# Kernel tuning notes

Measured on AMD Instinct MI355X. Metric: run time of the kernel, lower is better.

## Reference

```python
import jax, jax.numpy as jnp
import numpy as np

B, C, H, W = 16, 96, 96, 96
K, N, R, CR = 4, 8, 6, 12  # scan dirs, d_state, dt_rank, SE hidden


def channel_ln(x, g, b, eps=1e-6):
    # LayerNorm over channel dim (channel_first)
    mu = jnp.mean(x, axis=1, keepdims=True)
    var = jnp.var(x, axis=1, keepdims=True)
    return (x - mu) * jax.lax.rsqrt(var + eps) * g[None, :, None, None] + b[None, :, None, None]


def conv1x1(x, w, b):
    return jnp.einsum('bchw,dc->bdhw', x, w) + b[None, :, None, None]


def ss2d(x, xproj_w, dtproj_w, dtproj_b, A_logs, Ds, g, bta):
    # 4-direction selective scan (VMamba SS2D core). x: (B,C,H,W)
    Bq, Cq, Hq, Wq = x.shape
    L = Hq * Wq
    xf = x.reshape(Bq, Cq, L)
    xt = jnp.transpose(x, (0, 1, 3, 2)).reshape(Bq, Cq, L)
    xs = jnp.stack([xf, xt, xf[..., ::-1], xt[..., ::-1]], axis=1)  # (B,K,C,L)
    x_dbl = jnp.einsum('bkcl,kdc->bkdl', xs, xproj_w)  # (B,K,R+2N,L)
    dts, Bs, Cs = jnp.split(x_dbl, [R, R + N], axis=2)
    delta = jax.nn.softplus(jnp.einsum('bkrl,kcr->bkcl', dts, dtproj_w) + dtproj_b[None, :, :, None])
    A = -jnp.exp(A_logs)  # (K,C,N)
    u_t = jnp.moveaxis(xs, -1, 0)   # (L,B,K,C)
    d_t = jnp.moveaxis(delta, -1, 0)
    B_t = jnp.moveaxis(Bs, -1, 0)   # (L,B,K,N)
    C_t = jnp.moveaxis(Cs, -1, 0)
    h0 = jnp.zeros((Bq, K, Cq, N), x.dtype)

    @jax.checkpoint
    def step(h, inp):
        u, d, Bv, Cv = inp
        dA = jnp.exp(d[..., None] * A)                      # (B,K,C,N)
        h = dA * h + (d * u)[..., None] * Bv[:, :, None, :]
        return h, jnp.sum(h * Cv[:, :, None, :], axis=-1)   # (B,K,C)

    _, ys = jax.lax.scan(step, h0, (u_t, d_t, B_t, C_t))
    ys = jnp.moveaxis(ys, 0, -1) + Ds[None, :, :, None] * xs  # (B,K,C,L)

    def untrans(yk):
        return jnp.transpose(yk.reshape(Bq, Cq, Wq, Hq), (0, 1, 3, 2)).reshape(Bq, Cq, L)

    out = ys[:, 0] + untrans(ys[:, 1]) + ys[:, 2, :, ::-1] + untrans(ys[:, 3][..., ::-1])
    return channel_ln(out.reshape(Bq, Cq, Hq, Wq), g, bta)


def block_forward(x, ln_g, ln_b, p1_w, p1_b, p2in_w, p2in_b, dw_w, dw_b,
                  xproj_w, dtproj_w, dtproj_b, A_logs, Ds, ssln_g, ssln_b,
                  p2n_g, p2n_b, ca_w1, ca_b1, ca_w2, ca_b2, block_idx):
    h = channel_ln(x, ln_g, ln_b)
    a = jax.nn.silu(conv1x1(h, p1_w, p1_b))
    z = conv1x1(h, p2in_w, p2in_b)
    z = jax.lax.conv_general_dilated(z, dw_w, (1, 1), 'SAME',
                                     dimension_numbers=('NCHW', 'OIHW', 'NCHW'),
                                     feature_group_count=z.shape[1]) + dw_b[None, :, None, None]
    z = jax.nn.silu(z)
    if block_idx % 2 == 0:
        z = jnp.transpose(z, (0, 1, 3, 2))
    else:
        z = z[:, :, ::-1, ::-1]
    z = ss2d(z, xproj_w, dtproj_w, dtproj_b, A_logs, Ds, ssln_g, ssln_b)
    if block_idx % 2 == 0:
        z = jnp.transpose(z, (0, 1, 3, 2))
    else:
        z = z[:, :, ::-1, ::-1]
    z = channel_ln(z, p2n_g, p2n_b)
    y = a * z
    # channel attention (SE)
    s = jnp.mean(y, axis=(2, 3))  # (B,C)
    att = jax.nn.sigmoid(jnp.einsum('cr,br->bc', ca_w2,
                                    jax.nn.silu(jnp.einsum('rc,bc->br', ca_w1, s) + ca_b1)) + ca_b2)
    return x + y * att[:, :, None, None]


def local_mamba(x, params, block_idx):
    b, c, h, w = x.shape
    h2, w2 = h // 2, w // 2
    qs = jnp.stack([x[:, :, :h2, :w2], x[:, :, :h2, w2:],
                    x[:, :, h2:, :w2], x[:, :, h2:, w2:]])  # (4,B,C,h2,w2)
    fn = lambda q, *p: block_forward(q, *p, block_idx)
    outs = jax.vmap(fn)(qs, *params)
    top = jnp.concatenate([outs[0], outs[1]], axis=3)
    bot = jnp.concatenate([outs[2], outs[3]], axis=3)
    return jnp.concatenate([top, bot], axis=2)


def setup_inputs() -> dict:
    key = jax.random.key(0)
    ks = jax.random.split(key, 12)
    rn = lambda k, shape, s=1.0: jax.random.normal(k, shape, jnp.float32) * s
    return dict(
        x=rn(ks[0], (B, C, H, W)),
        ln_g=jnp.ones((4, C)), ln_b=jnp.zeros((4, C)),
        p1_w=rn(ks[1], (4, C, C), C ** -0.5), p1_b=jnp.zeros((4, C)),
        p2in_w=rn(ks[2], (4, C, C), C ** -0.5), p2in_b=jnp.zeros((4, C)),
        dw_w=rn(ks[3], (4, C, 1, 3, 3), 1.0 / 3.0), dw_b=jnp.zeros((4, C)),
        xproj_w=rn(ks[4], (4, K, R + 2 * N, C), C ** -0.5),
        dtproj_w=rn(ks[5], (4, K, C, R), R ** -0.5),
        dtproj_b=rn(ks[6], (4, K, C), 0.1),
        A_logs=jax.random.uniform(ks[7], (4, K, C, N), jnp.float32, 0.0, 1.0),
        Ds=jnp.ones((4, K, C)),
        ssln_g=jnp.ones((4, C)), ssln_b=jnp.zeros((4, C)),
        p2n_g=jnp.ones((4, C)), p2n_b=jnp.zeros((4, C)),
        ca_w1=rn(ks[8], (4, CR, C), C ** -0.5), ca_b1=jnp.zeros((4, CR)),
        ca_w2=rn(ks[9], (4, C, CR), CR ** -0.5), ca_b2=jnp.zeros((4, C)),
        block_idx=0,
    )


def reference(x, ln_g, ln_b, p1_w, p1_b, p2in_w, p2in_b, dw_w, dw_b,
              xproj_w, dtproj_w, dtproj_b, A_logs, Ds, ssln_g, ssln_b,
              p2n_g, p2n_b, ca_w1, ca_b1, ca_w2, ca_b2, block_idx):
    params = (ln_g, ln_b, p1_w, p1_b, p2in_w, p2in_b, dw_w, dw_b,
              xproj_w, dtproj_w, dtproj_b, A_logs, Ds, ssln_g, ssln_b,
              p2n_g, p2n_b, ca_w1, ca_b1, ca_w2, ca_b2)
    return local_mamba(x, params, block_idx)
```

## Files before the change

kernel.cpp:

```cpp
#include <hip/hip_runtime.h>
#include <hip/hip_bf16.h>

#define BQ 16
#define CN 96
#define HQ 48
#define LL 2304
#define NK 4
#define RR 6
#define NNS 8
#define DPJ 22
#define CRr 12
#define LOG2E 1.4426950408889634f

using bf16 = __hip_bfloat16;

__device__ __forceinline__ float b2f(bf16 v) { return __bfloat162float(v); }
__device__ __forceinline__ bf16  f2b(float v){ return __float2bfloat16(v); }
__device__ __forceinline__ float bflo(unsigned u){ return __uint_as_float(u << 16); }
__device__ __forceinline__ float bfhi(unsigned u){ return __uint_as_float(u & 0xffff0000u); }
__device__ __forceinline__ float sigf(float x){ return 1.f / (1.f + __expf(-x)); }
__device__ __forceinline__ float siluf(float x){ return x / (1.f + __expf(-x)); }
__device__ __forceinline__ unsigned packbf(float a, float b){
    unsigned lo = (unsigned)__builtin_bit_cast(unsigned short, f2b(a));
    unsigned hi = (unsigned)__builtin_bit_cast(unsigned short, f2b(b));
    return lo | (hi << 16);
}
__device__ __forceinline__ unsigned rot16(unsigned u){ return (u >> 16) | (u << 16); }
__device__ __forceinline__ void unpack8(uint4 v, float* f){
    f[0]=bflo(v.x); f[1]=bfhi(v.x); f[2]=bflo(v.y); f[3]=bfhi(v.y);
    f[4]=bflo(v.z); f[5]=bfhi(v.z); f[6]=bflo(v.w); f[7]=bfhi(v.w);
}
__device__ __forceinline__ void unpack4(uint2 v, float* f){
    f[0]=bflo(v.x); f[1]=bfhi(v.x); f[2]=bflo(v.y); f[3]=bfhi(v.y);
}
__device__ __forceinline__ float fexp2(float x){
#if __has_builtin(__builtin_amdgcn_exp2f)
    return __builtin_amdgcn_exp2f(x);
#else
    return __expf(x * 0.6931471805599453f);
#endif
}
__device__ __forceinline__ float qxor(float v, int ctrl_b1){
    int x;
    if (ctrl_b1) x = __builtin_amdgcn_mov_dpp(__float_as_int(v), 0xB1, 0xF, 0xF, true);
    else         x = __builtin_amdgcn_mov_dpp(__float_as_int(v), 0x4E, 0xF, 0xF, true);
    return __int_as_float(x);
}

__global__ __launch_bounds__(192) void k_lnconv(
    const float* __restrict__ x, const float* __restrict__ ln_g, const float* __restrict__ ln_b,
    const float* __restrict__ p1w, const float* __restrict__ p1b,
    const float* __restrict__ p2w, const float* __restrict__ p2b,
    bf16* __restrict__ a_out, bf16* __restrict__ z0_out)
{
    const int hh2 = blockIdx.x;
    const int b = blockIdx.y, q = blockIdx.z;
    const int h0 = (q >> 1) * HQ, w0 = (q & 1) * HQ;
    const int tid = threadIdx.x;
    const int qb = q * BQ + b;

    __shared__ alignas(16) bf16 hn[CN * 96];
    __shared__ alignas(16) bf16 wl[CN * 200];
    __shared__ float mu[96], rs[96];

    for (int t = tid; t < CN * CN; t += 192) {
        int d = t / CN, c = t % CN;
        wl[c * 200 + d]      = f2b(p1w[(q * CN + d) * CN + c]);
        wl[c * 200 + 96 + d] = f2b(p2w[(q * CN + d) * CN + c]);
    }
    for (int t = tid; t < CN * 24; t += 192) {
        int c = t / 24, v = t % 24;
        int row = v / 12, col = (v % 12) * 4;
        float4 xv = *reinterpret_cast<const float4*>(
            &x[((b * CN + c) * 96 + h0 + 2 * hh2 + row) * 96 + w0 + col]);
        uint2 pk; pk.x = packbf(xv.x, xv.y); pk.y = packbf(xv.z, xv.w);
        *reinterpret_cast<uint2*>(&hn[c * 96 + v * 4]) = pk;
    }
    __syncthreads();
    if (tid < 96) {
        float s = 0.f, s2 = 0.f;
        for (int c = 0; c < CN; ++c) { float v = b2f(hn[c * 96 + tid]); s += v; s2 += v * v; }
        float m = s * (1.f / 96.f);
        float var = s2 * (1.f / 96.f) - m * m;
        mu[tid] = m; rs[tid] = rsqrtf(var + 1e-6f);
    }
    __syncthreads();
    for (int t = tid; t < CN * 96; t += 192) {
        int c = t / 96, p = t % 96;
        float g = ln_g[q * CN + c], bb = ln_b[q * CN + c];
        hn[t] = f2b((b2f(hn[t]) - mu[p]) * rs[p] * g + bb);
    }
    __syncthreads();
    const int rg = tid >> 3, pg = tid & 7;
    const int row0 = rg * 8, pp0 = pg * 12;
    float acc[8][12];
    #pragma unroll
    for (int i = 0; i < 8; ++i)
        #pragma unroll
        for (int j = 0; j < 12; ++j) acc[i][j] = 0.f;

    for (int c = 0; c < CN; ++c) {
        uint4 wv = *reinterpret_cast<const uint4*>(&wl[c * 200 + row0]);
        float w[8];
        w[0] = bflo(wv.x); w[1] = bfhi(wv.x);
        w[2] = bflo(wv.y); w[3] = bfhi(wv.y);
        w[4] = bflo(wv.z); w[5] = bfhi(wv.z);
        w[6] = bflo(wv.w); w[7] = bfhi(wv.w);
        uint2 ha = *reinterpret_cast<const uint2*>(&hn[c * 96 + pp0]);
        uint2 hb = *reinterpret_cast<const uint2*>(&hn[c * 96 + pp0 + 4]);
        uint2 hc = *reinterpret_cast<const uint2*>(&hn[c * 96 + pp0 + 8]);
        float hv[12];
        hv[0] = bflo(ha.x); hv[1] = bfhi(ha.x); hv[2]  = bflo(ha.y); hv[3]  = bfhi(ha.y);
        hv[4] = bflo(hb.x); hv[5] = bfhi(hb.x); hv[6]  = bflo(hb.y); hv[7]  = bfhi(hb.y);
        hv[8] = bflo(hc.x); hv[9] = bfhi(hc.x); hv[10] = bflo(hc.y); hv[11] = bfhi(hc.y);
        #pragma unroll
        for (int i = 0; i < 8; ++i)
            #pragma unroll
            for (int j = 0; j < 12; ++j)
                acc[i][j] = fmaf(w[i], hv[j], acc[i][j]);
    }
    const int lbase = (2 * hh2 + pp0 / 48) * 48 + (pp0 % 48);
    #pragma unroll
    for (int i = 0; i < 8; ++i) {
        int row = row0 + i;
        bool isA = row < 96;
        int d = isA ? row : row - 96;
        float bias = isA ? p1b[q * CN + d] : p2b[q * CN + d];
        int oidx = (qb * CN + d) * LL + lbase;
        float v[12];
        #pragma unroll
        for (int j = 0; j < 12; ++j) v[j] = acc[i][j] + bias;
        if (isA) {
            #pragma unroll
            for (int j = 0; j < 12; ++j) v[j] = siluf(v[j]);
        }
        uint2 w0p, w1p, w2p;
        w0p.x = packbf(v[0], v[1]);  w0p.y = packbf(v[2], v[3]);
        w1p.x = packbf(v[4], v[5]);  w1p.y = packbf(v[6], v[7]);
        w2p.x = packbf(v[8], v[9]);  w2p.y = packbf(v[10], v[11]);
        bf16* dst = isA ? a_out : z0_out;
        *reinterpret_cast<uint2*>(&dst[oidx])     = w0p;
        *reinterpret_cast<uint2*>(&dst[oidx + 4]) = w1p;
        *reinterpret_cast<uint2*>(&dst[oidx + 8]) = w2p;
    }
}

__global__ __launch_bounds__(256) void k_dwconv(
    const bf16* __restrict__ z0, const float* __restrict__ dww, const float* __restrict__ dwb,
    const int* __restrict__ bidx, bf16* __restrict__ zt, bf16* __restrict__ ztT)
{
    const int c = blockIdx.x, b = blockIdx.y, q = blockIdx.z;
    const int tid = threadIdx.x;
    const int base = ((q * BQ + b) * CN + c) * LL;
    __shared__ float zin[LL];
    __shared__ float zo[48 * 49];
    for (int t = tid; t < 288; t += 256) {
        uint4 v = *reinterpret_cast<const uint4*>(&z0[base + t * 8]);
        float f[8]; unpack8(v, f);
        *reinterpret_cast<float4*>(&zin[t * 8])     = make_float4(f[0], f[1], f[2], f[3]);
        *reinterpret_cast<float4*>(&zin[t * 8 + 4]) = make_float4(f[4], f[5], f[6], f[7]);
    }
    float wk[9];
    #pragma unroll
    for (int i = 0; i < 9; ++i) wk[i] = dww[(q * CN + c) * 9 + i];
    const float bias = dwb[q * CN + c];
    __syncthreads();
    for (int t = tid; t < LL; t += 256) {
        int hh = t / 48, ww = t % 48;
        float s = bias;
        #pragma unroll
        for (int dy = -1; dy <= 1; ++dy)
            #pragma unroll
            for (int dx = -1; dx <= 1; ++dx) {
                int yy = hh + dy, xx = ww + dx;
                if (yy >= 0 && yy < 48 && xx >= 0 && xx < 48)
                    s = fmaf(wk[(dy + 1) * 3 + (dx + 1)], zin[yy * 48 + xx], s);
            }
        zo[hh * 49 + ww] = siluf(s);
    }
    __syncthreads();
    const bool even = ((bidx[0] & 1) == 0);
    for (int t = tid; t < LL; t += 256) {
        int i = t / 48, j = t % 48;
        float vz, vzT;
        if (even) { vz = zo[j * 49 + i];               vzT = zo[i * 49 + j]; }
        else      { vz = zo[(47 - i) * 49 + (47 - j)]; vzT = zo[(47 - j) * 49 + (47 - i)]; }
        zt[base + t]  = f2b(vz);
        ztT[base + t] = f2b(vzT);
    }
}

__global__ __launch_bounds__(256) void k_xdbl(
    const bf16* __restrict__ zt, const bf16* __restrict__ ztT,
    const float* __restrict__ xprojw, bf16* __restrict__ xdbl)
{
    const int lt = blockIdx.x, k = blockIdx.y, qb = blockIdx.z;
    const int tid = threadIdx.x;
    const int l0 = lt * 192;
    const int q = qb >> 4;
    __shared__ alignas(16) bf16 ul[CN * 200];
    __shared__ alignas(16) bf16 wl[CN * 24];
    const bf16* __restrict__ src = (k & 1) ? ztT : zt;
    const bool rev = (k >= 2);
    for (int t = tid; t < CN * 24; t += 256) {
        int cc = t / 24, j0 = (t % 24) * 8;
        uint4 v;
        if (!rev) {
            v = *reinterpret_cast<const uint4*>(&src[(size_t)(qb * CN + cc) * LL + l0 + j0]);
        } else {
            v = *reinterpret_cast<const uint4*>(&src[(size_t)(qb * CN + cc) * LL + (LL - (l0 + j0) - 8)]);
            uint4 r; r.x = rot16(v.w); r.y = rot16(v.z); r.z = rot16(v.y); r.w = rot16(v.x);
            v = r;
        }
        *reinterpret_cast<uint4*>(&ul[cc * 200 + j0]) = v;
    }
    for (int t = tid; t < DPJ * CN; t += 256) {
        int d = t / CN, c = t % CN;
        wl[c * 24 + d] = f2b(xprojw[(q * NK + k) * DPJ * CN + t]);
    }
    __syncthreads();
    if (tid < 176) {
        const int dp = tid / 16, lg = tid % 16;
        const int d0 = dp * 2, llp = lg * 12;
        float acc0[12], acc1[12];
        #pragma unroll
        for (int j = 0; j < 12; ++j) { acc0[j] = 0.f; acc1[j] = 0.f; }
        for (int c = 0; c < CN; ++c) {
            unsigned wv = *reinterpret_cast<const unsigned*>(&wl[c * 24 + d0]);
            float w0 = bflo(wv), w1 = bfhi(wv);
            uint2 ua = *reinterpret_cast<const uint2*>(&ul[c * 200 + llp]);
            uint2 ub = *reinterpret_cast<const uint2*>(&ul[c * 200 + llp + 4]);
            uint2 uc = *reinterpret_cast<const uint2*>(&ul[c * 200 + llp + 8]);
            float uf[12];
            unpack4(ua, uf); unpack4(ub, uf + 4); unpack4(uc, uf + 8);
            #pragma unroll
            for (int j = 0; j < 12; ++j) {
                acc0[j] = fmaf(w0, uf[j], acc0[j]);
                acc1[j] = fmaf(w1, uf[j], acc1[j]);
            }
        }
        int ob = (qb * NK + k) * DPJ * LL + l0 + llp;
        uint2 o0a, o0b, o0c, o1a, o1b, o1c;
        o0a.x = packbf(acc0[0], acc0[1]);  o0a.y = packbf(acc0[2], acc0[3]);
        o0b.x = packbf(acc0[4], acc0[5]);  o0b.y = packbf(acc0[6], acc0[7]);
        o0c.x = packbf(acc0[8], acc0[9]);  o0c.y = packbf(acc0[10], acc0[11]);
        o1a.x = packbf(acc1[0], acc1[1]);  o1a.y = packbf(acc1[2], acc1[3]);
        o1b.x = packbf(acc1[4], acc1[5]);  o1b.y = packbf(acc1[6], acc1[7]);
        o1c.x = packbf(acc1[8], acc1[9]);  o1c.y = packbf(acc1[10], acc1[11]);
        *reinterpret_cast<uint2*>(&xdbl[ob + d0 * LL])           = o0a;
        *reinterpret_cast<uint2*>(&xdbl[ob + d0 * LL + 4])       = o0b;
        *reinterpret_cast<uint2*>(&xdbl[ob + d0 * LL + 8])       = o0c;
        *reinterpret_cast<uint2*>(&xdbl[ob + (d0 + 1) * LL])     = o1a;
        *reinterpret_cast<uint2*>(&xdbl[ob + (d0 + 1) * LL + 4]) = o1b;
        *reinterpret_cast<uint2*>(&xdbl[ob + (d0 + 1) * LL + 8]) = o1c;
    }
}

__global__ __launch_bounds__(192) void k_scan(
    const bf16* __restrict__ zt, const bf16* __restrict__ ztT,
    const bf16* __restrict__ xdbl,
    const float* __restrict__ dtw_g, const float* __restrict__ dtb_g,
    const float* __restrict__ Alog_g, const float* __restrict__ Ds_g,
    bf16* __restrict__ ys)
{
    const int bid = blockIdx.x;
    const int ch2 = bid & 1, k = (bid >> 1) & 3, qb = bid >> 3, q = qb >> 4;
    const int qk = q * NK + k;
    const int tid = threadIdx.x;
    const int ca = tid >> 2, p = tid & 3;
    const int c = ch2 * 48 + ca;

    __shared__ float uu[2][48 * 52];
    __shared__ float dd[2][48 * 52];
    __shared__ float xr[2][6 * 52];
    __shared__ float bcv[2][48 * 16];

    const float* wp = dtw_g + (size_t)qk * CN * RR + c * RR;
    float wdt[6];
    {
        float2 wa = *reinterpret_cast<const float2*>(wp);
        float2 wb = *reinterpret_cast<const float2*>(wp + 2);
        float2 wc = *reinterpret_cast<const float2*>(wp + 4);
        wdt[0] = wa.x; wdt[1] = wa.y; wdt[2] = wb.x; wdt[3] = wb.y; wdt[4] = wc.x; wdt[5] = wc.y;
    }
    const float dtbc = dtb_g[qk * CN + c];
    const float A0L = -__expf(Alog_g[((size_t)qk * CN + c) * NNS + 2 * p])     * LOG2E;
    const float A1L = -__expf(Alog_g[((size_t)qk * CN + c) * NNS + 2 * p + 1]) * LOG2E;
    const float Dc = Ds_g[qk * CN + c];
    float h0 = 0.f, h1 = 0.f;

    const bf16* __restrict__ src = (k & 1) ? ztT : zt;
    const bool rev = (k >= 2);
    const int ja = p * 12;

    const bf16* gu = src + (size_t)(qb * CN + c) * LL + (rev ? (LL - 12 - ja) : ja);
    const int ustep = rev ? -48 : 48;

    const bool xload = (tid < 132);
    const int vr = tid / 6, jx = (tid % 6) * 8;
    const bf16* gx = xdbl + (size_t)(qb * NK + k) * (DPJ * LL) + (size_t)vr * LL + jx;
    int bccol = 0;
    if (vr >= 6) {
        int v = vr - 6;
        int n = v & 7;
        bccol = (n >> 1) * 4 + ((v >= 8) ? 2 : 0) + (n & 1);
    }

    bf16* yp = ys + (size_t)(qb * NK + k) * (CN * LL) + (size_t)c * LL;

    uint2 pu0 = *reinterpret_cast<const uint2*>(gu);
    uint2 pu1 = *reinterpret_cast<const uint2*>(gu + 4);
    uint2 pu2 = *reinterpret_cast<const uint2*>(gu + 8);
    uint4 px = {0,0,0,0};
    if (xload) px = *reinterpret_cast<const uint4*>(gx);

    {
        float e[12];
        unpack4(pu0, e); unpack4(pu1, e + 4); unpack4(pu2, e + 8);
        float f[12];
        #pragma unroll
        for (int i = 0; i < 12; ++i) f[i] = rev ? e[11 - i] : e[i];
        float4* up = reinterpret_cast<float4*>(&uu[0][ca * 52 + ja]);
        up[0] = make_float4(f[0], f[1], f[2], f[3]);
        up[1] = make_float4(f[4], f[5], f[6], f[7]);
        up[2] = make_float4(f[8], f[9], f[10], f[11]);
        if (xload) {
            float g[8]; unpack8(px, g);
            if (vr < 6) {
                *reinterpret_cast<float4*>(&xr[0][vr * 52 + jx])     = make_float4(g[0], g[1], g[2], g[3]);
                *reinterpret_cast<float4*>(&xr[0][vr * 52 + jx + 4]) = make_float4(g[4], g[5], g[6], g[7]);
            } else {
                #pragma unroll
                for (int i = 0; i < 8; ++i) bcv[0][(jx + i) * 16 + bccol] = g[i];
            }
        }
    }
    gu += ustep;
    pu0 = *reinterpret_cast<const uint2*>(gu);
    pu1 = *reinterpret_cast<const uint2*>(gu + 4);
    pu2 = *reinterpret_cast<const uint2*>(gu + 8);
    if (xload) { gx += 48; px = *reinterpret_cast<const uint4*>(gx); }
    __syncthreads();
    {
        float acc[12];
        #pragma unroll
        for (int i = 0; i < 12; ++i) acc[i] = dtbc;
        #pragma unroll
        for (int r = 0; r < 6; ++r) {
            float4 d0 = *reinterpret_cast<const float4*>(&xr[0][r * 52 + ja]);
            float4 d1 = *reinterpret_cast<const float4*>(&xr[0][r * 52 + ja + 4]);
            float4 d2 = *reinterpret_cast<const float4*>(&xr[0][r * 52 + ja + 8]);
            float w = wdt[r];
            acc[0] = fmaf(w, d0.x, acc[0]);  acc[1] = fmaf(w, d0.y, acc[1]);
            acc[2] = fmaf(w, d0.z, acc[2]);  acc[3] = fmaf(w, d0.w, acc[3]);
            acc[4] = fmaf(w, d1.x, acc[4]);  acc[5] = fmaf(w, d1.y, acc[5]);
            acc[6] = fmaf(w, d1.z, acc[6]);  acc[7] = fmaf(w, d1.w, acc[7]);
            acc[8] = fmaf(w, d2.x, acc[8]);  acc[9] = fmaf(w, d2.y, acc[9]);
            acc[10] = fmaf(w, d2.z, acc[10]); acc[11] = fmaf(w, d2.w, acc[11]);
        }
        #pragma unroll
        for (int i = 0; i < 12; ++i) {
            float a = acc[i];
            acc[i] = (a > 15.f) ? a : __logf(1.f + __expf(a));
        }
        float4* dp = reinterpret_cast<float4*>(&dd[0][ca * 52 + ja]);
        dp[0] = make_float4(acc[0], acc[1], acc[2], acc[3]);
        dp[1] = make_float4(acc[4], acc[5], acc[6], acc[7]);
        dp[2] = make_float4(acc[8], acc[9], acc[10], acc[11]);
    }
    __syncthreads();

    for (int ch = 0; ch < 48; ++ch) {
        const int cur = ch & 1, nxt = cur ^ 1;
        if (ch < 47) {
            float e[12];
            unpack4(pu0, e); unpack4(pu1, e + 4); unpack4(pu2, e + 8);
            float f[12];
            #pragma unroll
            for (int i = 0; i < 12; ++i) f[i] = rev ? e[11 - i] : e[i];
            float4* up = reinterpret_cast<float4*>(&uu[nxt][ca * 52 + ja]);
            up[0] = make_float4(f[0], f[1], f[2], f[3]);
            up[1] = make_float4(f[4], f[5], f[6], f[7]);
            up[2] = make_float4(f[8], f[9], f[10], f[11]);
            if (xload) {
                float g[8]; unpack8(px, g);
                if (vr < 6) {
                    *reinterpret_cast<float4*>(&xr[nxt][vr * 52 + jx])     = make_float4(g[0], g[1], g[2], g[3]);
                    *reinterpret_cast<float4*>(&xr[nxt][vr * 52 + jx + 4]) = make_float4(g[4], g[5], g[6], g[7]);
                } else {
                    #pragma unroll
                    for (int i = 0; i < 8; ++i) bcv[nxt][(jx + i) * 16 + bccol] = g[i];
                }
            }
        }
        __syncthreads();
        if (ch < 46) {
            gu += ustep;
            pu0 = *reinterpret_cast<const uint2*>(gu);
            pu1 = *reinterpret_cast<const uint2*>(gu + 4);
            pu2 = *reinterpret_cast<const uint2*>(gu + 8);
            if (xload) { gx += 48; px = *reinterpret_cast<const uint4*>(gx); }
        }
        if (ch < 47) {
            float acc[12];
            #pragma unroll
            for (int i = 0; i < 12; ++i) acc[i] = dtbc;
            #pragma unroll
            for (int r = 0; r < 6; ++r) {
                float4 d0 = *reinterpret_cast<const float4*>(&xr[nxt][r * 52 + ja]);
                float4 d1 = *reinterpret_cast<const float4*>(&xr[nxt][r * 52 + ja + 4]);
                float4 d2 = *reinterpret_cast<const float4*>(&xr[nxt][r * 52 + ja + 8]);
                float w = wdt[r];
                acc[0] = fmaf(w, d0.x, acc[0]);  acc[1] = fmaf(w, d0.y, acc[1]);
                acc[2] = fmaf(w, d0.z, acc[2]);  acc[3] = fmaf(w, d0.w, acc[3]);
                acc[4] = fmaf(w, d1.x, acc[4]);  acc[5] = fmaf(w, d1.y, acc[5]);
                acc[6] = fmaf(w, d1.z, acc[6]);  acc[7] = fmaf(w, d1.w, acc[7]);
                acc[8] = fmaf(w, d2.x, acc[8]);  acc[9] = fmaf(w, d2.y, acc[9]);
                acc[10] = fmaf(w, d2.z, acc[10]); acc[11] = fmaf(w, d2.w, acc[11]);
            }
            #pragma unroll
            for (int i = 0; i < 12; ++i) {
                float a = acc[i];
                acc[i] = (a > 15.f) ? a : __logf(1.f + __expf(a));
            }
            float4* dp = reinterpret_cast<float4*>(&dd[nxt][ca * 52 + ja]);
            dp[0] = make_float4(acc[0], acc[1], acc[2], acc[3]);
            dp[1] = make_float4(acc[4], acc[5], acc[6], acc[7]);
            dp[2] = make_float4(acc[8], acc[9], acc[10], acc[11]);
        }
        {
            const int l0 = ch * 48;
            const float* uuc = &uu[cur][ca * 52];
            const float* ddc = &dd[cur][ca * 52];
            const float* bcc = &bcv[cur][p * 4];
            #pragma unroll
            for (int gg = 0; gg < 6; ++gg) {
                unsigned pk[4];
                #pragma unroll
                for (int half = 0; half < 2; ++half) {
                    const int j0 = gg * 8 + half * 4;
                    float4 u4 = *reinterpret_cast<const float4*>(uuc + j0);
                    float4 d4 = *reinterpret_cast<const float4*>(ddc + j0);
                    const float* uf = reinterpret_cast<const float*>(&u4);
                    const float* df = reinterpret_cast<const float*>(&d4);
                    #pragma unroll
                    for (int s = 0; s < 4; ++s) {
                        float u = uf[s], d = df[s];
                        float4 bq = *reinterpret_cast<const float4*>(bcc + (j0 + s) * 16);
                        float du = d * u;
                        float dA0 = fexp2(d * A0L);
                        float dA1 = fexp2(d * A1L);
                        h0 = fmaf(dA0, h0, du * bq.x);
                        h1 = fmaf(dA1, h1, du * bq.y);
                        float y = fmaf(h0, bq.z, h1 * bq.w);
                        y += qxor(y, 1); y += qxor(y, 0);
                        y = fmaf(Dc, u, y);
                        unsigned hb = (unsigned)__builtin_bit_cast(unsigned short, f2b(y));
                        const int sl = half * 4 + s;
                        if (sl & 1) pk[sl >> 1] |= hb << 16; else pk[sl >> 1] = hb;
                    }
                }
                if (p == 0) {
                    uint4 w; w.x = pk[0]; w.y = pk[1]; w.z = pk[2]; w.w = pk[3];
                    *reinterpret_cast<uint4*>(yp + l0 + gg * 8) = w;
                }
            }
        }
        __syncthreads();
    }
}

__global__ __launch_bounds__(256) void k_sum(
    const bf16* __restrict__ ys, bf16* __restrict__ s_out)
{
    const int c = blockIdx.x, b = blockIdx.y, q = blockIdx.z;
    const int qb = q * BQ + b;
    const int tid = threadIdx.x;
    __shared__ float t0[48 * 49];
    __shared__ float t2[48 * 49];
    const size_t base0 = ((size_t)(qb * NK + 0) * CN + c) * LL;
    const size_t base1 = ((size_t)(qb * NK + 1) * CN + c) * LL;
    const size_t base2 = ((size_t)(qb * NK + 2) * CN + c) * LL;
    const size_t base3 = ((size_t)(qb * NK + 3) * CN + c) * LL;
    for (int idx = tid; idx < 288; idx += 256) {
        int e0 = idx * 8, h = e0 / 48, w = e0 % 48;
        float f[8];
        unpack8(*reinterpret_cast<const uint4*>(&ys[base0 + e0]), f);
        #pragma unroll
        for (int i = 0; i < 8; ++i) t0[h * 49 + w + i] = f[i];
        unpack8(*reinterpret_cast<const uint4*>(&ys[base2 + e0]), f);
        #pragma unroll
        for (int i = 0; i < 8; ++i) t2[h * 49 + w + i] = f[i];
    }
    __syncthreads();
    const size_t cbase = ((size_t)qb * CN + c) * LL;
    for (int idx = tid; idx < 288; idx += 256) {
        int m0 = idx * 8, ww = m0 / 48, hh = m0 % 48;
        float f1[8], f3[8];
        unpack8(*reinterpret_cast<const uint4*>(&ys[base1 + m0]), f1);
        unpack8(*reinterpret_cast<const uint4*>(&ys[base3 + (LL - 8 - m0)]), f3);
        float o[8];
        #pragma unroll
        for (int i = 0; i < 8; ++i) {
            float v0 = t0[(hh + i) * 49 + ww];
            float v2 = t2[(47 - hh - i) * 49 + (47 - ww)];
            o[i] = v0 + f1[i] + v2 + f3[7 - i];
        }
        uint4 w;
        w.x = packbf(o[0], o[1]); w.y = packbf(o[2], o[3]);
        w.z = packbf(o[4], o[5]); w.w = packbf(o[6], o[7]);
        *reinterpret_cast<uint4*>(&s_out[cbase + m0]) = w;
    }
}

__global__ __launch_bounds__(256) void k_combine(
    const bf16* __restrict__ s_in, const bf16* __restrict__ a_in,
    const float* __restrict__ ssg, const float* __restrict__ ssb,
    const float* __restrict__ png, const float* __restrict__ pnb,
    const int* __restrict__ bidx,
    bf16* __restrict__ y_out, float* __restrict__ s_buf)
{
    const int ww = blockIdx.x, b = blockIdx.y, q = blockIdx.z;
    const int qb = q * BQ + b;
    const int tid = threadIdx.x;
    __shared__ float o[CN * 48];
    __shared__ float mu[48], rs[48];
    for (int v = tid; v < 576; v += 256) {
        int e0 = v * 8, cc = e0 / 48, hh = e0 % 48;
        float f[8];
        unpack8(*reinterpret_cast<const uint4*>(&s_in[((size_t)qb * CN + cc) * LL + ww * 48 + hh]), f);
        #pragma unroll
        for (int i = 0; i < 8; ++i) o[cc * 48 + hh + i] = f[i];
    }
    __syncthreads();
    if (tid < 48) {
        float s = 0.f, s2 = 0.f;
        for (int cc = 0; cc < CN; ++cc) { float v = o[cc * 48 + tid]; s += v; s2 += v * v; }
        float m = s * (1.f / 96.f), var = s2 * (1.f / 96.f) - m * m;
        mu[tid] = m; rs[tid] = rsqrtf(var + 1e-6f);
    }
    __syncthreads();
    for (int t = tid; t < CN * 48; t += 256) {
        int cc = t / 48, hh = t % 48;
        o[t] = (o[t] - mu[hh]) * rs[hh] * ssg[q * CN + cc] + ssb[q * CN + cc];
    }
    __syncthreads();
    if (tid < 48) {
        float s = 0.f, s2 = 0.f;
        for (int cc = 0; cc < CN; ++cc) { float v = o[cc * 48 + tid]; s += v; s2 += v * v; }
        float m = s * (1.f / 96.f), var = s2 * (1.f / 96.f) - m * m;
        mu[tid] = m; rs[tid] = rsqrtf(var + 1e-6f);
    }
    __syncthreads();
    const bool even = ((bidx[0] & 1) == 0);
    if (even) {
        for (int v = tid; v < 576; v += 256) {
            int e0 = v * 8, cc = e0 / 48, hh = e0 % 48;
            size_t oidx = ((size_t)qb * CN + cc) * LL + ww * 48 + hh;
            float af[8];
            unpack8(*reinterpret_cast<const uint4*>(&a_in[oidx]), af);
            float yv[8];
            #pragma unroll
            for (int i = 0; i < 8; ++i) {
                float z2 = (o[cc * 48 + hh + i] - mu[hh + i]) * rs[hh + i] * png[q * CN + cc] + pnb[q * CN + cc];
                yv[i] = af[i] * z2;
                o[cc * 48 + hh + i] = yv[i];
            }
            uint4 w;
            w.x = packbf(yv[0], yv[1]); w.y = packbf(yv[2], yv[3]);
            w.z = packbf(yv[4], yv[5]); w.w = packbf(yv[6], yv[7]);
            *reinterpret_cast<uint4*>(&y_out[oidx]) = w;
        }
    } else {
        for (int t = tid; t < CN * 48; t += 256) {
            int cc = t / 48, hh = t % 48;
            float z2 = (o[t] - mu[hh]) * rs[hh] * png[q * CN + cc] + pnb[q * CN + cc];
            size_t oidx = ((size_t)qb * CN + cc) * LL + (47 - hh) * 48 + (47 - ww);
            float yv = b2f(a_in[oidx]) * z2;
            y_out[oidx] = f2b(yv);
            o[t] = yv;
        }
    }
    __syncthreads();
    if (tid < CN) {
        float s = 0.f;
        for (int j = 0; j < 48; ++j) s += o[tid * 48 + j];
        atomicAdd(&s_buf[qb * CN + tid], s);
    }
}

__global__ __launch_bounds__(256) void k_final(
    const float* __restrict__ x, const bf16* __restrict__ y_in,
    const float* __restrict__ s_buf,
    const float* __restrict__ w1, const float* __restrict__ b1,
    const float* __restrict__ w2, const float* __restrict__ b2,
    float* __restrict__ out)
{
    const int c = blockIdx.x, b = blockIdx.y, q = blockIdx.z;
    const int h0 = (q >> 1) * HQ, w0 = (q & 1) * HQ;
    const int qb = q * BQ + b;
    const int tid = threadIdx.x;
    __shared__ float tl[CRr];
    __shared__ float attv;
    if (tid < CRr) {
        float acc = b1[q * CRr + tid];
        const float* wr = w1 + (q * CRr + tid) * CN;
        const float* sb = s_buf + qb * CN;
        for (int cc = 0; cc < CN; ++cc)
            acc = fmaf(wr[cc], sb[cc] * (1.f / (float)LL), acc);
        tl[tid] = siluf(acc);
    }
    __syncthreads();
    if (tid == 0) {
        float acc = b2[q * CN + c];
        #pragma unroll
        for (int r = 0; r < CRr; ++r) acc = fmaf(w2[(q * CN + c) * CRr + r], tl[r], acc);
        attv = sigf(acc);
    }
    __syncthreads();
    const float av = attv;
    const size_t ybase = (size_t)(qb * CN + c) * LL;
    const int xb = (b * CN + c) * 9216 + h0 * 96 + w0;
    for (int t = tid; t < LL / 8; t += 256) {
        int e0 = t * 8;
        int gi = xb + (e0 / 48) * 96 + (e0 % 48);
        uint4 yv = *reinterpret_cast<const uint4*>(&y_in[ybase + e0]);
        float yf[8]; unpack8(yv, yf);
        float4 xa = *reinterpret_cast<const float4*>(&x[gi]);
        float4 xc = *reinterpret_cast<const float4*>(&x[gi + 4]);
        float4 o0 = {xa.x + yf[0]*av, xa.y + yf[1]*av, xa.z + yf[2]*av, xa.w + yf[3]*av};
        float4 o1 = {xc.x + yf[4]*av, xc.y + yf[5]*av, xc.z + yf[6]*av, xc.w + yf[7]*av};
        *reinterpret_cast<float4*>(&out[gi])     = o0;
        *reinterpret_cast<float4*>(&out[gi + 4]) = o1;
    }
}

extern "C" void kernel_launch(void* const* d_in, const int* in_sizes, int n_in,
                              void* d_out, int out_size, void* d_ws, size_t ws_size,
                              hipStream_t stream)
{
    (void)in_sizes; (void)n_in; (void)out_size; (void)ws_size;
    const float* x       = (const float*)d_in[0];
    const float* ln_g    = (const float*)d_in[1];
    const float* ln_b    = (const float*)d_in[2];
    const float* p1_w    = (const float*)d_in[3];
    const float* p1_b    = (const float*)d_in[4];
    const float* p2in_w  = (const float*)d_in[5];
    const float* p2in_b  = (const float*)d_in[6];
    const float* dw_w    = (const float*)d_in[7];
    const float* dw_b    = (const float*)d_in[8];
    const float* xproj_w = (const float*)d_in[9];
    const float* dtproj_w= (const float*)d_in[10];
    const float* dtproj_b= (const float*)d_in[11];
    const float* A_logs  = (const float*)d_in[12];
    const float* Ds      = (const float*)d_in[13];
    const float* ssln_g  = (const float*)d_in[14];
    const float* ssln_b  = (const float*)d_in[15];
    const float* p2n_g   = (const float*)d_in[16];
    const float* p2n_b   = (const float*)d_in[17];
    const float* ca_w1   = (const float*)d_in[18];
    const float* ca_b1   = (const float*)d_in[19];
    const float* ca_w2   = (const float*)d_in[20];
    const float* ca_b2   = (const float*)d_in[21];
    const int*  bidx     = (const int*)d_in[22];
    float* out = (float*)d_out;

    char* ws = (char*)d_ws;
    const size_t off_a    = 0;
    const size_t off_zt   = 28311552;
    const size_t off_ztT  = 56623104;
    const size_t off_xdbl = 84934656;
    const size_t off_ys   = 110886912;
    const size_t off_z0   = off_ys;
    const size_t off_s    = off_zt;
    const size_t off_y    = off_ztT;
    const size_t off_sb   = 224133120;

    bf16*  a_buf   = (bf16*)(ws + off_a);
    bf16*  zt_buf  = (bf16*)(ws + off_zt);
    bf16*  ztT_buf = (bf16*)(ws + off_ztT);
    bf16*  xdbl_buf= (bf16*)(ws + off_xdbl);
    bf16*  ys_buf  = (bf16*)(ws + off_ys);
    bf16*  z0_buf  = (bf16*)(ws + off_z0);
    bf16*  s_sum   = (bf16*)(ws + off_s);
    bf16*  y_buf   = (bf16*)(ws + off_y);
    float* s_buf   = (float*)(ws + off_sb);

    (void)hipMemsetAsync(ws + off_sb, 0, 24576, stream);

    k_lnconv<<<dim3(24, 16, 4), 192, 0, stream>>>(
        x, ln_g, ln_b, p1_w, p1_b, p2in_w, p2in_b, a_buf, z0_buf);
    k_dwconv<<<dim3(96, 16, 4), 256, 0, stream>>>(
        z0_buf, dw_w, dw_b, bidx, zt_buf, ztT_buf);
    k_xdbl<<<dim3(12, 4, 64), 256, 0, stream>>>(
        zt_buf, ztT_buf, xproj_w, xdbl_buf);
    k_scan<<<dim3(512), 192, 0, stream>>>(
        zt_buf, ztT_buf, xdbl_buf, dtproj_w, dtproj_b, A_logs, Ds, ys_buf);
    k_sum<<<dim3(96, 16, 4), 256, 0, stream>>>(
        ys_buf, s_sum);
    k_combine<<<dim3(48, 16, 4), 256, 0, stream>>>(
        s_sum, a_buf, ssln_g, ssln_b, p2n_g, p2n_b, bidx, y_buf, s_buf);
    k_final<<<dim3(96, 16, 4), 256, 0, stream>>>(
        x, y_buf, s_buf, ca_w1, ca_b1, ca_w2, ca_b2, out);
}
```

Measured before the change: 734.9 us.

## Keep scan inputs in registers and triple-buffer LDS with one barrier per chunk

```diff
diff --git a/kernel.cpp b/kernel.cpp
--- a/kernel.cpp
+++ b/kernel.cpp
@@ -256,6 +256,13 @@
     }
 }
 
+
+#define SCAN_BARRIER() asm volatile("s_waitcnt lgkmcnt(0)\n\ts_barrier" ::: "memory")
+
+#define UWORD(NUA, IDX) (((IDX) & 3) == 0 ? NUA[(IDX) >> 2].x : \
+                         ((IDX) & 3) == 1 ? NUA[(IDX) >> 2].y : \
+                         ((IDX) & 3) == 2 ? NUA[(IDX) >> 2].z : NUA[(IDX) >> 2].w)
+
 __global__ __launch_bounds__(192) void k_scan(
     const bf16* __restrict__ zt, const bf16* __restrict__ ztT,
     const bf16* __restrict__ xdbl,
@@ -270,10 +277,9 @@
     const int ca = tid >> 2, p = tid & 3;
     const int c = ch2 * 48 + ca;
 
-    __shared__ float uu[2][48 * 52];
-    __shared__ float dd[2][48 * 52];
-    __shared__ float xr[2][6 * 52];
-    __shared__ float bcv[2][48 * 16];
+    __shared__ float dd3[3][48 * 52];
+    __shared__ float xr3[3][6 * 52];
+    __shared__ float bcv3[3][48 * 16];
 
     const float* wp = dtw_g + (size_t)qk * CN * RR + c * RR;
     float wdt[6];
@@ -293,7 +299,7 @@
     const bool rev = (k >= 2);
     const int ja = p * 12;
 
-    const bf16* gu = src + (size_t)(qb * CN + c) * LL + (rev ? (LL - 12 - ja) : ja);
+    const bf16* gu = src + (size_t)(qb * CN + c) * LL + (rev ? (LL - 48) : 0);
     const int ustep = rev ? -48 : 48;
 
     const bool xload = (tid < 132);
@@ -308,166 +314,150 @@
 
     bf16* yp = ys + (size_t)(qb * NK + k) * (CN * LL) + (size_t)c * LL;
 
-    uint2 pu0 = *reinterpret_cast<const uint2*>(gu);
-    uint2 pu1 = *reinterpret_cast<const uint2*>(gu + 4);
-    uint2 pu2 = *reinterpret_cast<const uint2*>(gu + 8);
-    uint4 px = {0,0,0,0};
-    if (xload) px = *reinterpret_cast<const uint4*>(gx);
-
-    {
-        float e[12];
-        unpack4(pu0, e); unpack4(pu1, e + 4); unpack4(pu2, e + 8);
-        float f[12];
-        #pragma unroll
-        for (int i = 0; i < 12; ++i) f[i] = rev ? e[11 - i] : e[i];
-        float4* up = reinterpret_cast<float4*>(&uu[0][ca * 52 + ja]);
-        up[0] = make_float4(f[0], f[1], f[2], f[3]);
-        up[1] = make_float4(f[4], f[5], f[6], f[7]);
-        up[2] = make_float4(f[8], f[9], f[10], f[11]);
-        if (xload) {
-            float g[8]; unpack8(px, g);
-            if (vr < 6) {
-                *reinterpret_cast<float4*>(&xr[0][vr * 52 + jx])     = make_float4(g[0], g[1], g[2], g[3]);
-                *reinterpret_cast<float4*>(&xr[0][vr * 52 + jx + 4]) = make_float4(g[4], g[5], g[6], g[7]);
-            } else {
-                #pragma unroll
-                for (int i = 0; i < 8; ++i) bcv[0][(jx + i) * 16 + bccol] = g[i];
-            }
-        }
-    }
+    uint4 px0 = {0,0,0,0};
+    if (xload) px0 = *reinterpret_cast<const uint4*>(gx);
+    uint4 u_a[6], u_b[6];
+    #pragma unroll
+    for (int i = 0; i < 6; ++i) u_a[i] = *reinterpret_cast<const uint4*>(gu + i * 8);
     gu += ustep;
-    pu0 = *reinterpret_cast<const uint2*>(gu);
-    pu1 = *reinterpret_cast<const uint2*>(gu + 4);
-    pu2 = *reinterpret_cast<const uint2*>(gu + 8);
-    if (xload) { gx += 48; px = *reinterpret_cast<const uint4*>(gx); }
-    __syncthreads();
-    {
-        float acc[12];
-        #pragma unroll
-        for (int i = 0; i < 12; ++i) acc[i] = dtbc;
-        #pragma unroll
-        for (int r = 0; r < 6; ++r) {
-            float4 d0 = *reinterpret_cast<const float4*>(&xr[0][r * 52 + ja]);
-            float4 d1 = *reinterpret_cast<const float4*>(&xr[0][r * 52 + ja + 4]);
-            float4 d2 = *reinterpret_cast<const float4*>(&xr[0][r * 52 + ja + 8]);
-            float w = wdt[r];
-            acc[0] = fmaf(w, d0.x, acc[0]);  acc[1] = fmaf(w, d0.y, acc[1]);
-            acc[2] = fmaf(w, d0.z, acc[2]);  acc[3] = fmaf(w, d0.w, acc[3]);
-            acc[4] = fmaf(w, d1.x, acc[4]);  acc[5] = fmaf(w, d1.y, acc[5]);
-            acc[6] = fmaf(w, d1.z, acc[6]);  acc[7] = fmaf(w, d1.w, acc[7]);
-            acc[8] = fmaf(w, d2.x, acc[8]);  acc[9] = fmaf(w, d2.y, acc[9]);
-            acc[10] = fmaf(w, d2.z, acc[10]); acc[11] = fmaf(w, d2.w, acc[11]);
-        }
-        #pragma unroll
-        for (int i = 0; i < 12; ++i) {
-            float a = acc[i];
-            acc[i] = (a > 15.f) ? a : __logf(1.f + __expf(a));
-        }
-        float4* dp = reinterpret_cast<float4*>(&dd[0][ca * 52 + ja]);
-        dp[0] = make_float4(acc[0], acc[1], acc[2], acc[3]);
-        dp[1] = make_float4(acc[4], acc[5], acc[6], acc[7]);
-        dp[2] = make_float4(acc[8], acc[9], acc[10], acc[11]);
-    }
-    __syncthreads();
-
-    for (int ch = 0; ch < 48; ++ch) {
-        const int cur = ch & 1, nxt = cur ^ 1;
-        if (ch < 47) {
-            float e[12];
-            unpack4(pu0, e); unpack4(pu1, e + 4); unpack4(pu2, e + 8);
-            float f[12];
-            #pragma unroll
-            for (int i = 0; i < 12; ++i) f[i] = rev ? e[11 - i] : e[i];
-            float4* up = reinterpret_cast<float4*>(&uu[nxt][ca * 52 + ja]);
-            up[0] = make_float4(f[0], f[1], f[2], f[3]);
-            up[1] = make_float4(f[4], f[5], f[6], f[7]);
-            up[2] = make_float4(f[8], f[9], f[10], f[11]);
-            if (xload) {
-                float g[8]; unpack8(px, g);
-                if (vr < 6) {
-                    *reinterpret_cast<float4*>(&xr[nxt][vr * 52 + jx])     = make_float4(g[0], g[1], g[2], g[3]);
-                    *reinterpret_cast<float4*>(&xr[nxt][vr * 52 + jx + 4]) = make_float4(g[4], g[5], g[6], g[7]);
-                } else {
-                    #pragma unroll
-                    for (int i = 0; i < 8; ++i) bcv[nxt][(jx + i) * 16 + bccol] = g[i];
-                }
-            }
-        }
-        __syncthreads();
-        if (ch < 46) {
-            gu += ustep;
-            pu0 = *reinterpret_cast<const uint2*>(gu);
-            pu1 = *reinterpret_cast<const uint2*>(gu + 4);
-            pu2 = *reinterpret_cast<const uint2*>(gu + 8);
-            if (xload) { gx += 48; px = *reinterpret_cast<const uint4*>(gx); }
-        }
-        if (ch < 47) {
-            float acc[12];
-            #pragma unroll
-            for (int i = 0; i < 12; ++i) acc[i] = dtbc;
-            #pragma unroll
-            for (int r = 0; r < 6; ++r) {
-                float4 d0 = *reinterpret_cast<const float4*>(&xr[nxt][r * 52 + ja]);
-                float4 d1 = *reinterpret_cast<const float4*>(&xr[nxt][r * 52 + ja + 4]);
-                float4 d2 = *reinterpret_cast<const float4*>(&xr[nxt][r * 52 + ja + 8]);
-                float w = wdt[r];
-                acc[0] = fmaf(w, d0.x, acc[0]);  acc[1] = fmaf(w, d0.y, acc[1]);
-                acc[2] = fmaf(w, d0.z, acc[2]);  acc[3] = fmaf(w, d0.w, acc[3]);
-                acc[4] = fmaf(w, d1.x, acc[4]);  acc[5] = fmaf(w, d1.y, acc[5]);
-                acc[6] = fmaf(w, d1.z, acc[6]);  acc[7] = fmaf(w, d1.w, acc[7]);
-                acc[8] = fmaf(w, d2.x, acc[8]);  acc[9] = fmaf(w, d2.y, acc[9]);
-                acc[10] = fmaf(w, d2.z, acc[10]); acc[11] = fmaf(w, d2.w, acc[11]);
-            }
-            #pragma unroll
-            for (int i = 0; i < 12; ++i) {
-                float a = acc[i];
-                acc[i] = (a > 15.f) ? a : __logf(1.f + __expf(a));
-            }
-            float4* dp = reinterpret_cast<float4*>(&dd[nxt][ca * 52 + ja]);
-            dp[0] = make_float4(acc[0], acc[1], acc[2], acc[3]);
-            dp[1] = make_float4(acc[4], acc[5], acc[6], acc[7]);
-            dp[2] = make_float4(acc[8], acc[9], acc[10], acc[11]);
-        }
-        {
-            const int l0 = ch * 48;
-            const float* uuc = &uu[cur][ca * 52];
-            const float* ddc = &dd[cur][ca * 52];
-            const float* bcc = &bcv[cur][p * 4];
-            #pragma unroll
-            for (int gg = 0; gg < 6; ++gg) {
-                unsigned pk[4];
-                #pragma unroll
-                for (int half = 0; half < 2; ++half) {
-                    const int j0 = gg * 8 + half * 4;
-                    float4 u4 = *reinterpret_cast<const float4*>(uuc + j0);
-                    float4 d4 = *reinterpret_cast<const float4*>(ddc + j0);
-                    const float* uf = reinterpret_cast<const float*>(&u4);
-                    const float* df = reinterpret_cast<const float*>(&d4);
-                    #pragma unroll
-                    for (int s = 0; s < 4; ++s) {
-                        float u = uf[s], d = df[s];
-                        float4 bq = *reinterpret_cast<const float4*>(bcc + (j0 + s) * 16);
-                        float du = d * u;
-                        float dA0 = fexp2(d * A0L);
-                        float dA1 = fexp2(d * A1L);
-                        h0 = fmaf(dA0, h0, du * bq.x);
-                        h1 = fmaf(dA1, h1, du * bq.y);
-                        float y = fmaf(h0, bq.z, h1 * bq.w);
-                        y += qxor(y, 1); y += qxor(y, 0);
-                        y = fmaf(Dc, u, y);
-                        unsigned hb = (unsigned)__builtin_bit_cast(unsigned short, f2b(y));
-                        const int sl = half * 4 + s;
-                        if (sl & 1) pk[sl >> 1] |= hb << 16; else pk[sl >> 1] = hb;
-                    }
-                }
-                if (p == 0) {
-                    uint4 w; w.x = pk[0]; w.y = pk[1]; w.z = pk[2]; w.w = pk[3];
-                    *reinterpret_cast<uint4*>(yp + l0 + gg * 8) = w;
-                }
-            }
-        }
-        __syncthreads();
-    }
+    #pragma unroll
+    for (int i = 0; i < 6; ++i) u_b[i] = *reinterpret_cast<const uint4*>(gu + i * 8);
+    gu += ustep;
+    uint4 px_a = {0,0,0,0}, px_b = {0,0,0,0};
+    if (xload) {
+        px_a = *reinterpret_cast<const uint4*>(gx + 48);
+        px_b = *reinterpret_cast<const uint4*>(gx + 96);
+        gx += 144;
+    }
+
+    #define COMMIT_BLOCK(PXV, XRB, BCB) do {                                          \
+        if (xload) {                                                                  \
+            float g[8]; unpack8(PXV, g);                                              \
+            if (vr < 6) {                                                             \
+                *reinterpret_cast<float4*>(&(XRB)[vr * 52 + jx])                      \
+                    = make_float4(g[0], g[1], g[2], g[3]);                            \
+                *reinterpret_cast<float4*>(&(XRB)[vr * 52 + jx + 4])                  \
+                    = make_float4(g[4], g[5], g[6], g[7]);                            \
+            } else {                                                                  \
+                _Pragma("unroll")                                                     \
+                for (int i = 0; i < 8; ++i) (BCB)[(jx + i) * 16 + bccol] = g[i];      \
+            }                                                                         \
+        }                                                                             \
+    } while (0)
+
+    #define DELTA_BLOCK(XRB, DDB) do {                                                \
+        float acc[12];                                                                \
+        _Pragma("unroll")                                                             \
+        for (int i = 0; i < 12; ++i) acc[i] = dtbc;                                   \
+        _Pragma("unroll")                                                             \
+        for (int r = 0; r < 6; ++r) {                                                 \
+            float4 d0 = *reinterpret_cast<const float4*>(&(XRB)[r * 52 + ja]);        \
+            float4 d1 = *reinterpret_cast<const float4*>(&(XRB)[r * 52 + ja + 4]);    \
+            float4 d2 = *reinterpret_cast<const float4*>(&(XRB)[r * 52 + ja + 8]);    \
+            float wr_ = wdt[r];                                                       \
+            acc[0] = fmaf(wr_, d0.x, acc[0]);  acc[1] = fmaf(wr_, d0.y, acc[1]);      \
+            acc[2] = fmaf(wr_, d0.z, acc[2]);  acc[3] = fmaf(wr_, d0.w, acc[3]);      \
+            acc[4] = fmaf(wr_, d1.x, acc[4]);  acc[5] = fmaf(wr_, d1.y, acc[5]);      \
+            acc[6] = fmaf(wr_, d1.z, acc[6]);  acc[7] = fmaf(wr_, d1.w, acc[7]);      \
+            acc[8] = fmaf(wr_, d2.x, acc[8]);  acc[9] = fmaf(wr_, d2.y, acc[9]);      \
+            acc[10] = fmaf(wr_, d2.z, acc[10]); acc[11] = fmaf(wr_, d2.w, acc[11]);   \
+        }                                                                             \
+        _Pragma("unroll")                                                             \
+        for (int i = 0; i < 12; ++i) {                                                \
+            float a = acc[i];                                                         \
+            acc[i] = (a > 15.f) ? a : __logf(1.f + __expf(a));                        \
+        }                                                                             \
+        float4* dp = reinterpret_cast<float4*>(&(DDB)[ca * 52 + ja]);                 \
+        dp[0] = make_float4(acc[0], acc[1], acc[2], acc[3]);                          \
+        dp[1] = make_float4(acc[4], acc[5], acc[6], acc[7]);                          \
+        dp[2] = make_float4(acc[8], acc[9], acc[10], acc[11]);                        \
+    } while (0)
+
+    COMMIT_BLOCK(px0, xr3[0], bcv3[0]);
+    SCAN_BARRIER();
+    DELTA_BLOCK(xr3[0], dd3[0]);
+
+    int b_cur = 0, b_nxt = 1, b_thd = 2;
+
+    #define SCAN_BODY(CH, UC, PX) do {                                                \
+        const int ch_ = (CH);                                                         \
+                     \
+        uint4 nu[6];                                                                  \
+        if (!rev) {                                                                   \
+            nu[0] = UC[0]; nu[1] = UC[1]; nu[2] = UC[2];                              \
+            nu[3] = UC[3]; nu[4] = UC[4]; nu[5] = UC[5];                              \
+        } else {                                                                      \
+            _Pragma("unroll")                                                         \
+            for (int qq = 0; qq < 6; ++qq) {                                          \
+                nu[qq].x = rot16(UC[5 - qq].w); nu[qq].y = rot16(UC[5 - qq].z);       \
+                nu[qq].z = rot16(UC[5 - qq].y); nu[qq].w = rot16(UC[5 - qq].x);       \
+            }                                                                         \
+        }                                                                             \
+                                          \
+        if (ch_ < 47) COMMIT_BLOCK(PX, xr3[b_nxt], bcv3[b_nxt]);                      \
+                      \
+        if (ch_ < 45 && xload) { PX = *reinterpret_cast<const uint4*>(gx); gx += 48; }\
+                                      \
+        SCAN_BARRIER();                                                               \
+                          \
+        if (ch_ < 47) DELTA_BLOCK(xr3[b_nxt], dd3[b_nxt]);                            \
+                                                                \
+        {                                                                             \
+            const int l0 = ch_ * 48;                                                  \
+            const float* ddc = &dd3[b_cur][ca * 52];                                  \
+            const float* bcc = &bcv3[b_cur][p * 4];                                   \
+            _Pragma("unroll")                                                         \
+            for (int gg = 0; gg < 6; ++gg) {                                          \
+                unsigned pk[4];                                                       \
+                _Pragma("unroll")                                                     \
+                for (int half = 0; half < 2; ++half) {                                \
+                    const int j0 = gg * 8 + half * 4;                                 \
+                    float4 d4 = *reinterpret_cast<const float4*>(ddc + j0);           \
+                    const float* df = reinterpret_cast<const float*>(&d4);            \
+                    _Pragma("unroll")                                                 \
+                    for (int s = 0; s < 4; ++s) {                                     \
+                        const int j = j0 + s;                                         \
+                        const unsigned uwv = UWORD(nu, j >> 1);                       \
+                        float u = (j & 1) ? bfhi(uwv) : bflo(uwv);                    \
+                        float d = df[s];                                              \
+                        float4 bq = *reinterpret_cast<const float4*>(bcc + j * 16);   \
+                        float du = d * u;                                             \
+                        float dA0 = fexp2(d * A0L);                                   \
+                        float dA1 = fexp2(d * A1L);                                   \
+                        h0 = fmaf(dA0, h0, du * bq.x);                                \
+                        h1 = fmaf(dA1, h1, du * bq.y);                                \
+                        float y = fmaf(h0, bq.z, h1 * bq.w);                          \
+                        y += qxor(y, 1); y += qxor(y, 0);                             \
+                        y = fmaf(Dc, u, y);                                           \
+                        unsigned hb = (unsigned)__builtin_bit_cast(unsigned short, f2b(y)); \
+                        const int sl = half * 4 + s;                                  \
+                        if (sl & 1) pk[sl >> 1] |= hb << 16; else pk[sl >> 1] = hb;   \
+                    }                                                                 \
+                }                                                                     \
+                if (p == 0) {                                                         \
+                    uint4 wv4; wv4.x = pk[0]; wv4.y = pk[1]; wv4.z = pk[2]; wv4.w = pk[3]; \
+                    *reinterpret_cast<uint4*>(yp + l0 + gg * 8) = wv4;                \
+                }                                                                     \
+            }                                                                         \
+        }                                                                             \
+                    \
+        if (ch_ < 46) {                                                               \
+            _Pragma("unroll")                                                         \
+            for (int i = 0; i < 6; ++i) UC[i] = *reinterpret_cast<const uint4*>(gu + i * 8); \
+            gu += ustep;                                                              \
+        }                                                                             \
+                                                               \
+        { int tb = b_cur; b_cur = b_nxt; b_nxt = b_thd; b_thd = tb; }                 \
+    } while (0)
+
+    for (int t = 0; t < 24; ++t) {
+        SCAN_BODY(2 * t,     u_a, px_a);
+        SCAN_BODY(2 * t + 1, u_b, px_b);
+    }
+
+    #undef SCAN_BODY
+    #undef DELTA_BLOCK
+    #undef COMMIT_BLOCK
 }
 
 __global__ __launch_bounds__(256) void k_sum(
```

Result: no change. 736.8 us (+0.3%).
